# Optimization experiments

Hardware: AMD Instinct MI355X
Metric: run time of the kernel (lower is better)

## Reference

```python
import jax, jax.numpy as jnp
import numpy as np

H = 8  # num_heads
NEG = -1e6  # mask fill value used by the torch masked_softmax


def layernorm(x, g, b, eps=1e-5):
    mu = jnp.mean(x, axis=-1, keepdims=True)
    var = jnp.mean(jnp.square(x - mu), axis=-1, keepdims=True)
    return (x - mu) * jax.lax.rsqrt(var + eps) * g + b


def setup_inputs() -> dict:
    key = jax.random.key(0)
    ks = jax.random.split(key, 10)
    B, S, D, F = 8, 1024, 512, 2048
    s = 0.02
    return {
        "X": jax.random.normal(ks[0], (B, S, D), jnp.float32),
        "valid_lens": jax.random.randint(ks[1], (B,), 1, S + 1, jnp.int32),
        "ln1_g": jnp.ones((D,), jnp.float32),
        "ln1_b": jnp.zeros((D,), jnp.float32),
        "Wq": jax.random.normal(ks[2], (D, D), jnp.float32) * s,
        "Wk": jax.random.normal(ks[3], (D, D), jnp.float32) * s,
        "Wv": jax.random.normal(ks[4], (D, D), jnp.float32) * s,
        "Wo": jax.random.normal(ks[5], (D, D), jnp.float32) * s,
        "ln2_g": jnp.ones((D,), jnp.float32),
        "ln2_b": jnp.zeros((D,), jnp.float32),
        "W1": jax.random.normal(ks[6], (D, F), jnp.float32) * s,
        "b1": jnp.zeros((F,), jnp.float32),
        "W2": jax.random.normal(ks[7], (F, D), jnp.float32) * s,
        "b2": jnp.zeros((D,), jnp.float32),
    }


def vit_block(X, valid_lens, ln1_g, ln1_b, Wq, Wk, Wv, Wo, ln2_g, ln2_b, W1, b1, W2, b2):
    B, S, D = X.shape
    dh = D // H
    h = layernorm(X, ln1_g, ln1_b)
    # project and split heads: [B, S, H, dh]
    q = (h @ Wq).reshape(B, S, H, dh)
    k = (h @ Wk).reshape(B, S, H, dh)
    v = (h @ Wv).reshape(B, S, H, dh)
    scores = jnp.einsum("bqhd,bkhd->bhqk", q, k) / jnp.sqrt(jnp.float32(dh))
    # mask keys >= valid_len[b] with -1e6 (as in masked_softmax)
    mask = jnp.arange(S)[None, None, None, :] < valid_lens[:, None, None, None]
    scores = jnp.where(mask, scores, NEG)
    attn = jax.nn.softmax(scores, axis=-1)
    out = jnp.einsum("bhqk,bkhd->bqhd", attn, v).reshape(B, S, D)
    X = X + out @ Wo
    h2 = layernorm(X, ln2_g, ln2_b)
    mlp = jax.nn.gelu(h2 @ W1 + b1, approximate=False) @ W2 + b2
    return X + mlp


def reference(X, valid_lens, ln1_g, ln1_b, Wq, Wk, Wv, Wo, ln2_g, ln2_b, W1, b1, W2, b2):
    return vit_block(X, valid_lens, ln1_g, ln1_b, Wq, Wk, Wv, Wo, ln2_g, ln2_b, W1, b1, W2, b2)
```

## Files before the change

kernel.cpp:

```cpp
#include <hip/hip_runtime.h>
#include <math.h>

#define BB 8
#define SS 1024
#define DD 512
#define FF 2048
#define NH 8
#define MM (BB * SS)
#define LDQKV 1536

using bf8 = __attribute__((ext_vector_type(8))) short;
using f4  = __attribute__((ext_vector_type(4))) float;

#define AS1 __attribute__((address_space(1)))
#define AS3 __attribute__((address_space(3)))

__device__ __forceinline__ void gload16(const void* g, void* l) {
  __builtin_amdgcn_global_load_lds((AS1 const void*)g, (AS3 void*)l, 16, 0, 0);
}

__device__ __forceinline__ unsigned short f2b(float f) {
  union { float f; unsigned u; } v; v.f = f;
  unsigned r = v.u + 0x7fffu + ((v.u >> 16) & 1u);
  return (unsigned short)(r >> 16);
}

__global__ __launch_bounds__(256) void ln_bf16(const float* __restrict__ x,
                                               const float* __restrict__ g,
                                               const float* __restrict__ bta,
                                               unsigned short* __restrict__ out) {
  int wave = threadIdx.x >> 6, lane = threadIdx.x & 63;
  int row = (blockIdx.x << 2) + wave;
  const float* xr = x + (size_t)row * DD;
  int base = lane << 3;
  float4 v0 = *(const float4*)(xr + base);
  float4 v1 = *(const float4*)(xr + base + 4);
  float s  = v0.x + v0.y + v0.z + v0.w + v1.x + v1.y + v1.z + v1.w;
  float sq = v0.x*v0.x + v0.y*v0.y + v0.z*v0.z + v0.w*v0.w
           + v1.x*v1.x + v1.y*v1.y + v1.z*v1.z + v1.w*v1.w;
  for (int m = 32; m; m >>= 1) { s += __shfl_xor(s, m); sq += __shfl_xor(sq, m); }
  float mu  = s * (1.0f / DD);
  float var = sq * (1.0f / DD) - mu * mu;
  float rs  = rsqrtf(var + 1e-5f);
  float xv[8], go[8], bo[8];
  *(float4*)(xv) = v0; *(float4*)(xv + 4) = v1;
  *(float4*)(go)     = *(const float4*)(g + base);
  *(float4*)(go + 4) = *(const float4*)(g + base + 4);
  *(float4*)(bo)     = *(const float4*)(bta + base);
  *(float4*)(bo + 4) = *(const float4*)(bta + base + 4);
  union { unsigned short u[8]; uint4 v; } ov;
#pragma unroll
  for (int i = 0; i < 8; i++) ov.u[i] = f2b((xv[i] - mu) * rs * go[i] + bo[i]);
  *(uint4*)(out + (size_t)row * DD + base) = ov.v;
}

__global__ __launch_bounds__(256) void tconv(const float* __restrict__ in,
                                             unsigned short* __restrict__ outp,
                                             int K, int N) {
  __shared__ float tile[32][33];
  int n0 = blockIdx.x << 5, k0 = blockIdx.y << 5;
  int c = threadIdx.x & 31, r = threadIdx.x >> 5;
#pragma unroll
  for (int i = 0; i < 4; i++)
    tile[r + 8 * i][c] = in[(size_t)(k0 + r + 8 * i) * N + n0 + c];
  __syncthreads();
#pragma unroll
  for (int i = 0; i < 4; i++)
    outp[(size_t)(n0 + r + 8 * i) * K + k0 + c] = f2b(tile[c][r + 8 * i]);
}

template <int BM, int BN, int ACT>
__global__ __launch_bounds__(256) void gemm_t(
    const unsigned short* __restrict__ A,
    const unsigned short* __restrict__ Bt,
    const float* __restrict__ bias,
    const float* __restrict__ res,
    float* __restrict__ Cf,
    unsigned short* __restrict__ Cb,
    int M, int N, int K) {
  constexpr int WM = BM / 2, WN = BN / 2;
  constexpr int FM = WM / 16, FN = WN / 16;
  constexpr int ACH = BM / 32, BCH = BN / 32;
  __shared__ unsigned short As[2][BM * 64];
  __shared__ unsigned short Bs[2][BN * 64];
  int tid = threadIdx.x, wid = tid >> 6, lane = tid & 63;
  int m0 = blockIdx.y * BM, n0 = blockIdx.x * BN;
  int wm = (wid >> 1) * WM, wn = (wid & 1) * WN;
  int r4 = lane & 15, ksl = lane >> 4;
  int srow = lane >> 3, gs = (lane & 7) ^ srow;

  const unsigned short* aBase =
      A + (size_t)(m0 + wid * (ACH * 8) + srow) * K + gs * 8;
  const unsigned short* bBase =
      Bt + (size_t)(n0 + wid * (BCH * 8) + srow) * K + gs * 8;

  f4 acc[FM][FN];
#pragma unroll
  for (int i = 0; i < FM; i++)
#pragma unroll
    for (int j = 0; j < FN; j++) acc[i][j] = (f4){0.f, 0.f, 0.f, 0.f};

  auto STAGE = [&](int buf, int k0) {
#pragma unroll
    for (int i = 0; i < ACH; i++)
      gload16(aBase + (size_t)i * 8 * K + k0, &As[buf][(wid * ACH + i) * 512]);
#pragma unroll
    for (int i = 0; i < BCH; i++)
      gload16(bBase + (size_t)i * 8 * K + k0, &Bs[buf][(wid * BCH + i) * 512]);
  };

  int nt = K >> 6;
  STAGE(0, 0);
  __syncthreads();
  int cur = 0;
  for (int t = 0; t < nt; t++) {
    if (t + 1 < nt) STAGE(cur ^ 1, (t + 1) << 6);
#pragma unroll
    for (int k2 = 0; k2 < 2; k2++) {
      bf8 af[FM], bfr[FN];
#pragma unroll
      for (int mi = 0; mi < FM; mi++) {
        int r = wm + mi * 16 + r4;
        af[mi] = *(const bf8*)((const char*)&As[cur][0] + r * 128 +
                               (((k2 * 4 + ksl) ^ (r & 7)) << 4));
      }
#pragma unroll
      for (int ni = 0; ni < FN; ni++) {
        int r = wn + ni * 16 + r4;
        bfr[ni] = *(const bf8*)((const char*)&Bs[cur][0] + r * 128 +
                                (((k2 * 4 + ksl) ^ (r & 7)) << 4));
      }
#pragma unroll
      for (int mi = 0; mi < FM; mi++)
#pragma unroll
        for (int ni = 0; ni < FN; ni++)
          acc[mi][ni] = __builtin_amdgcn_mfma_f32_16x16x32_bf16(
              af[mi], bfr[ni], acc[mi][ni], 0, 0, 0);
    }
    __syncthreads();
    cur ^= 1;
  }

  int rq = (lane >> 4) << 2;
#pragma unroll
  for (int ni = 0; ni < FN; ni++) {
    int col = n0 + wn + ni * 16 + r4;
    float bv = bias ? bias[col] : 0.0f;
#pragma unroll
    for (int mi = 0; mi < FM; mi++) {
#pragma unroll
      for (int j = 0; j < 4; j++) {
        int row = m0 + wm + mi * 16 + rq + j;
        float v = acc[mi][ni][j] + bv;
        if (ACT) v = 0.5f * v * (1.0f + erff(v * 0.70710678118654752f));
        if (res) v += res[(size_t)row * N + col];
        if (Cf) Cf[(size_t)row * N + col] = v;
        else    Cb[(size_t)row * N + col] = f2b(v);
      }
    }
  }
}

__global__ __launch_bounds__(256) void attn_mfma(
    const unsigned short* __restrict__ QKV,
    const int* __restrict__ vlen,
    unsigned short* __restrict__ AO) {
  __shared__ unsigned short Qs[64 * 64];
  __shared__ unsigned short Ks[64 * 64];
  __shared__ unsigned short Vt[64 * 64];
  __shared__ unsigned short Ps[64 * 64];
  int b = blockIdx.z, h = blockIdx.y, q0 = blockIdx.x << 6;
  int tid = threadIdx.x, wid = tid >> 6, lane = tid & 63;
  int vl = vlen[b];
  int r4 = lane & 15, ksl = lane >> 4;

  int srow = lane >> 3;
  int gs = (lane & 7) ^ srow;
  {
    const unsigned short* qsrc =
        QKV + (size_t)(b * SS + q0 + wid * 16 + srow) * LDQKV + h * 64 + gs * 8;
    gload16(qsrc, Qs + wid * 1024);
    gload16(qsrc + (size_t)8 * LDQKV, Qs + wid * 1024 + 512);
  }
  const unsigned short* kbase =
      QKV + (size_t)(b * SS + wid * 16 + srow) * LDQKV + DD + h * 64 + gs * 8;
  int vp = tid & 31, vdg = (tid >> 5) << 3;
  const unsigned short* vbase =
      QKV + (size_t)(b * SS + 2 * vp) * LDQKV + 2 * DD + h * 64 + vdg;

  f4 o[4];
#pragma unroll
  for (int i = 0; i < 4; i++) o[i] = (f4){0.f, 0.f, 0.f, 0.f};
  float mrun[4], lrun[4];
#pragma unroll
  for (int j = 0; j < 4; j++) { mrun[j] = -3e38f; lrun[j] = 0.0f; }

  int ntiles = (vl + 63) >> 6;
  if (ntiles > 16) ntiles = 16;

  for (int t = 0; t < ntiles; t++) {
    int kg0 = t << 6;
    const unsigned short* ks = kbase + (size_t)kg0 * LDQKV;
    gload16(ks, Ks + wid * 1024);
    gload16(ks + (size_t)8 * LDQKV, Ks + wid * 1024 + 512);
    {
      const unsigned short* v0 = vbase + (size_t)kg0 * LDQKV;
      const unsigned short* v1 = v0 + LDQKV;
      unsigned short va[8], vb[8];
      *(uint4*)va = *(const uint4*)v0;
      *(uint4*)vb = *(const uint4*)v1;
#pragma unroll
      for (int i = 0; i < 8; i++) {
        int d = vdg + i;
        unsigned val = (unsigned)va[i] | ((unsigned)vb[i] << 16);
        int byte = (d << 7) + (((vp >> 2) ^ (d & 7)) << 4) + ((vp & 3) << 2);
        *(unsigned*)((char*)Vt + byte) = val;
      }
    }
    __syncthreads();

    f4 s[4];
#pragma unroll
    for (int i = 0; i < 4; i++) s[i] = (f4){0.f, 0.f, 0.f, 0.f};
#pragma unroll
    for (int k2 = 0; k2 < 2; k2++) {
      int slot = (k2 << 2) + ksl;
      int qr = (wid << 4) + r4;
      bf8 aq = *(const bf8*)((const char*)Qs + (qr << 7) + ((slot ^ (qr & 7)) << 4));
#pragma unroll
      for (int ni = 0; ni < 4; ni++) {
        int kr = (ni << 4) + r4;
        bf8 bk = *(const bf8*)((const char*)Ks + (kr << 7) + ((slot ^ (kr & 7)) << 4));
        s[ni] = __builtin_amdgcn_mfma_f32_16x16x32_bf16(aq, bk, s[ni], 0, 0, 0);
      }
    }

#pragma unroll
    for (int j = 0; j < 4; j++) {
      int qr = (wid << 4) + ((lane >> 4) << 2) + j;
      float sv[4], mx = -3e38f;
#pragma unroll
      for (int ni = 0; ni < 4; ni++) {
        float v = s[ni][j] * 0.125f;
        if (kg0 + (ni << 4) + r4 >= vl) v = -1e6f;
        sv[ni] = v;
        mx = fmaxf(mx, v);
      }
#pragma unroll
      for (int m2 = 1; m2 < 16; m2 <<= 1) mx = fmaxf(mx, __shfl_xor(mx, m2));
      float mnew = fmaxf(mrun[j], mx);
      float al = __expf(mrun[j] - mnew);
      float ls = 0.0f;
      unsigned short pb[4];
#pragma unroll
      for (int ni = 0; ni < 4; ni++) {
        float p = __expf(sv[ni] - mnew);
        ls += p;
        pb[ni] = f2b(p);
      }
#pragma unroll
      for (int m2 = 1; m2 < 16; m2 <<= 1) ls += __shfl_xor(ls, m2);
      lrun[j] = lrun[j] * al + ls;
      mrun[j] = mnew;
#pragma unroll
      for (int ni = 0; ni < 4; ni++) {
        int kc = (ni << 4) + r4;
        int byte = (qr << 7) + (((kc >> 3) ^ (qr & 7)) << 4) + ((kc & 7) << 1);
        *(unsigned short*)((char*)Ps + byte) = pb[ni];
        o[ni][j] *= al;
      }
    }

#pragma unroll
    for (int k2 = 0; k2 < 2; k2++) {
      int slot = (k2 << 2) + ksl;
      int qr = (wid << 4) + r4;
      bf8 ap = *(const bf8*)((const char*)Ps + (qr << 7) + ((slot ^ (qr & 7)) << 4));
#pragma unroll
      for (int ni = 0; ni < 4; ni++) {
        int dr = (ni << 4) + r4;
        bf8 bv = *(const bf8*)((const char*)Vt + (dr << 7) + ((slot ^ (dr & 7)) << 4));
        o[ni] = __builtin_amdgcn_mfma_f32_16x16x32_bf16(ap, bv, o[ni], 0, 0, 0);
      }
    }
    __syncthreads();
  }

  float inv[4];
#pragma unroll
  for (int j = 0; j < 4; j++) inv[j] = 1.0f / lrun[j];
#pragma unroll
  for (int ni = 0; ni < 4; ni++) {
#pragma unroll
    for (int j = 0; j < 4; j++) {
      int qr = (wid << 4) + ((lane >> 4) << 2) + j;
      int d = (ni << 4) + r4;
      AO[(size_t)(b * SS + q0 + qr) * DD + h * 64 + d] = f2b(o[ni][j] * inv[j]);
    }
  }
}

extern "C" void kernel_launch(void* const* d_in, const int* in_sizes, int n_in,
                              void* d_out, int out_size, void* d_ws,
                              size_t ws_size, hipStream_t stream) {
  const float* X    = (const float*)d_in[0];
  const int*   vln  = (const int*)d_in[1];
  const float* ln1g = (const float*)d_in[2];
  const float* ln1b = (const float*)d_in[3];
  const float* Wq   = (const float*)d_in[4];
  const float* Wk   = (const float*)d_in[5];
  const float* Wv   = (const float*)d_in[6];
  const float* Wo   = (const float*)d_in[7];
  const float* ln2g = (const float*)d_in[8];
  const float* ln2b = (const float*)d_in[9];
  const float* W1   = (const float*)d_in[10];
  const float* b1   = (const float*)d_in[11];
  const float* W2   = (const float*)d_in[12];
  const float* b2   = (const float*)d_in[13];
  float* out = (float*)d_out;

  unsigned short* ws = (unsigned short*)d_ws;
  unsigned short* h     = ws;
  unsigned short* QKVb  = h     + (size_t)MM * DD;
  unsigned short* AOb   = QKVb  + (size_t)MM * LDQKV;
  unsigned short* mid   = AOb   + (size_t)MM * DD;
  unsigned short* Wqkvt = mid   + (size_t)MM * FF;
  unsigned short* Wot   = Wqkvt + (size_t)3 * DD * DD;
  unsigned short* W1t   = Wot   + (size_t)DD * DD;
  unsigned short* W2t   = W1t   + (size_t)FF * DD;

  dim3 blk(256);

  tconv<<<dim3(16, 16), blk, 0, stream>>>(Wq, Wqkvt, DD, DD);
  tconv<<<dim3(16, 16), blk, 0, stream>>>(Wk, Wqkvt + (size_t)DD * DD, DD, DD);
  tconv<<<dim3(16, 16), blk, 0, stream>>>(Wv, Wqkvt + (size_t)2 * DD * DD, DD, DD);
  tconv<<<dim3(16, 16), blk, 0, stream>>>(Wo, Wot, DD, DD);
  tconv<<<dim3(64, 16), blk, 0, stream>>>(W1, W1t, DD, FF);
  tconv<<<dim3(16, 64), blk, 0, stream>>>(W2, W2t, FF, DD);

  ln_bf16<<<dim3(MM / 4), blk, 0, stream>>>(X, ln1g, ln1b, h);
  gemm_t<128, 128, 0><<<dim3(LDQKV / 128, MM / 128), blk, 0, stream>>>(
      h, Wqkvt, nullptr, nullptr, nullptr, QKVb, MM, LDQKV, DD);
  attn_mfma<<<dim3(SS / 64, NH, BB), blk, 0, stream>>>(QKVb, vln, AOb);
  gemm_t<128, 64, 0><<<dim3(DD / 64, MM / 128), blk, 0, stream>>>(
      AOb, Wot, nullptr, X, out, nullptr, MM, DD, DD);
  ln_bf16<<<dim3(MM / 4), blk, 0, stream>>>(out, ln2g, ln2b, h);
  gemm_t<128, 128, 1><<<dim3(FF / 128, MM / 128), blk, 0, stream>>>(
      h, W1t, b1, nullptr, nullptr, mid, MM, FF, DD);
  gemm_t<128, 64, 0><<<dim3(DD / 64, MM / 128), blk, 0, stream>>>(
      mid, W2t, b2, out, out, nullptr, MM, DD, FF);
}
```

Baseline: 213.9 us.

## Prefetch two tiles ahead with explicit vmcnt waits in GEMM mainloop

Restructures the GEMM K-loop so two stages are in flight at once. Each iteration waits with s_waitcnt vmcnt only for the older tile instead of draining every outstanding global-to-LDS load at the barrier. The goal is to keep more memory latency hidden behind MFMA work. It adds a second barrier per iteration and hard-coded vmcnt values that must match ACH+BCH for each tile shape, which makes the code fragile.

```diff
diff --git a/kernel.cpp b/kernel.cpp
--- a/kernel.cpp
+++ b/kernel.cpp
@@ -17,6 +17,21 @@
 
 __device__ __forceinline__ void gload16(const void* g, void* l) {
   __builtin_amdgcn_global_load_lds((AS1 const void*)g, (AS3 void*)l, 16, 0, 0);
+}
+
+template <int N> __device__ __forceinline__ void wait_vm() {
+  if constexpr (N == 0)      asm volatile("s_waitcnt vmcnt(0)" ::: "memory");
+  else if constexpr (N == 4) asm volatile("s_waitcnt vmcnt(4)" ::: "memory");
+  else if constexpr (N == 6) asm volatile("s_waitcnt vmcnt(6)" ::: "memory");
+  else if constexpr (N == 8) asm volatile("s_waitcnt vmcnt(8)" ::: "memory");
+  else                       asm volatile("s_waitcnt vmcnt(12)" ::: "memory");
+  __builtin_amdgcn_sched_barrier(0);
+}
+
+__device__ __forceinline__ void bar() {
+  __builtin_amdgcn_sched_barrier(0);
+  __builtin_amdgcn_s_barrier();
+  __builtin_amdgcn_sched_barrier(0);
 }
 
 __device__ __forceinline__ unsigned short f2b(float f) {
@@ -81,6 +96,7 @@
   constexpr int WM = BM / 2, WN = BN / 2;
   constexpr int FM = WM / 16, FN = WN / 16;
   constexpr int ACH = BM / 32, BCH = BN / 32;
+  constexpr int L = ACH + BCH;
   __shared__ unsigned short As[2][BM * 64];
   __shared__ unsigned short Bs[2][BN * 64];
   int tid = threadIdx.x, wid = tid >> 6, lane = tid & 63;
@@ -100,7 +116,8 @@
 #pragma unroll
     for (int j = 0; j < FN; j++) acc[i][j] = (f4){0.f, 0.f, 0.f, 0.f};
 
-  auto STAGE = [&](int buf, int k0) {
+  auto STAGE = [&](int buf, int t) {
+    int k0 = t << 6;
 #pragma unroll
     for (int i = 0; i < ACH; i++)
       gload16(aBase + (size_t)i * 8 * K + k0, &As[buf][(wid * ACH + i) * 512]);
@@ -109,25 +126,20 @@
       gload16(bBase + (size_t)i * 8 * K + k0, &Bs[buf][(wid * BCH + i) * 512]);
   };
 
-  int nt = K >> 6;
-  STAGE(0, 0);
-  __syncthreads();
-  int cur = 0;
-  for (int t = 0; t < nt; t++) {
-    if (t + 1 < nt) STAGE(cur ^ 1, (t + 1) << 6);
+  auto COMPUTE = [&](int buf) {
 #pragma unroll
     for (int k2 = 0; k2 < 2; k2++) {
       bf8 af[FM], bfr[FN];
 #pragma unroll
       for (int mi = 0; mi < FM; mi++) {
         int r = wm + mi * 16 + r4;
-        af[mi] = *(const bf8*)((const char*)&As[cur][0] + r * 128 +
+        af[mi] = *(const bf8*)((const char*)&As[buf][0] + r * 128 +
                                (((k2 * 4 + ksl) ^ (r & 7)) << 4));
       }
 #pragma unroll
       for (int ni = 0; ni < FN; ni++) {
         int r = wn + ni * 16 + r4;
-        bfr[ni] = *(const bf8*)((const char*)&Bs[cur][0] + r * 128 +
+        bfr[ni] = *(const bf8*)((const char*)&Bs[buf][0] + r * 128 +
                                 (((k2 * 4 + ksl) ^ (r & 7)) << 4));
       }
 #pragma unroll
@@ -137,8 +149,18 @@
           acc[mi][ni] = __builtin_amdgcn_mfma_f32_16x16x32_bf16(
               af[mi], bfr[ni], acc[mi][ni], 0, 0, 0);
     }
-    __syncthreads();
-    cur ^= 1;
+  };
+
+  int nt = K >> 6;
+  STAGE(0, 0);
+  STAGE(1, 1);
+  for (int t = 0; t < nt; t++) {
+    if (t + 1 < nt) wait_vm<L>();
+    else            wait_vm<0>();
+    bar();
+    COMPUTE(t & 1);
+    bar();
+    if (t + 2 < nt) STAGE(t & 1, t + 2);
   }
 
   int rq = (lane >> 4) << 2;
```

After: 211.9 us. No clear change (-0.9%).
